# Kernel optimization log

Hardware: AMD Instinct MI355X
Metric: run time of the kernel (lower is better)

Reference implementation:

```python
import jax, jax.numpy as jnp
import numpy as np

N = 100000          # nodes
E = 600000          # edges
H = 128             # hidden_dim
CF_DIM = 15         # input_dim - 1
NOISE_DIM = 32
NUM_CLASS = 6       # GraphConstructor.number_of_class
B = 64              # number of graphs in batch
BC = B * NUM_CLASS  # total clusters
LAYER_NUM = 3
NEG_SLOPE = 0.01


def setup_inputs() -> dict:
    key = jax.random.key(0)
    ks = jax.random.split(key, 12)
    cf = jax.random.normal(ks[0], (N, CF_DIM), jnp.float32)
    slf = jax.random.uniform(ks[1], (N,), jnp.float32)
    z = jax.random.normal(ks[2], (N, NOISE_DIM), jnp.float32)
    tr = jax.random.uniform(ks[3], (BC,), jnp.float32)
    W_enc = jax.random.normal(ks[4], (CF_DIM + 1 + NOISE_DIM, H), jnp.float32) * 0.05
    b_enc = jax.random.normal(ks[5], (H,), jnp.float32) * 0.05
    W_m = jax.random.normal(ks[6], (2 * H, H), jnp.float32) * 0.05
    b_m = jax.random.normal(ks[7], (H,), jnp.float32) * 0.05
    W_u = jax.random.normal(ks[8], (3 * H, H), jnp.float32) * 0.05
    b_u = jax.random.normal(ks[9], (H,), jnp.float32) * 0.05
    e = jax.random.randint(ks[10], (2, E), 0, N, jnp.int64)
    cc = jax.random.randint(ks[11], (N,), 0, BC, jnp.int64)
    cfb = cc // NUM_CLASS  # batch index consistent with global cluster index
    return {"cf": cf, "slf": slf, "z": z, "tr": tr,
            "W_enc": W_enc, "b_enc": b_enc, "W_m": W_m, "b_m": b_m,
            "W_u": W_u, "b_u": b_u, "e": e, "cc": cc, "cfb": cfb}


def _segment_mean(x, idx, num_segments):
    s = jax.ops.segment_sum(x, idx, num_segments=num_segments)
    c = jax.ops.segment_sum(jnp.ones((x.shape[0],), x.dtype), idx, num_segments=num_segments)
    return s / jnp.maximum(c, 1.0)[:, None]


def reference(cf, slf, z, tr, W_enc, b_enc, W_m, b_m, W_u, b_u, e, cc, cfb):
    # encoder: x = enc(cat(cf, slf, z))  (Linear, no activation since act='')
    x = jnp.concatenate([cf, slf[:, None], z], axis=-1) @ W_enc + b_enc  # [N, H]
    src, dst = e[0], e[1]  # PyG: x_j = x[src], x_i = x[dst], aggregate at dst
    for _ in range(LAYER_NUM):
        # message: MLP(cat(feature_i, feature_j)) per edge, mean-aggregated at dst
        msg = jnp.concatenate([x[dst], x[src]], axis=-1) @ W_m + b_m  # [E, H]
        aggr = _segment_mean(msg, dst, N)                              # [N, H]
        # cluster avg_pool scaled by target ratio, broadcast back to nodes
        pooled = _segment_mean(x, cc, BC) * tr[:, None]                # [BC, H]
        node_pool = pooled[cc]                                         # [N, H]
        upd = jnp.concatenate([x, aggr, node_pool], axis=-1) @ W_u + b_u
        upd = jnp.where(upd > 0, upd, NEG_SLOPE * upd)                 # LeakyReLU
        x = x + upd                                                    # residual
    return x
```

## Files before the change

### kernel.cpp

```cpp
#include <hip/hip_runtime.h>
#include <hip/hip_bf16.h>

#define N_NODES 100000
#define N_EDGES 600000
#define HD 128
#define NBC 384
#define SCAN_B 98
#define MAXFIX 4096
#define TILES ((N_NODES + 63) / 64)
#define GRID_F 512
#define AGG_B (N_NODES / 4)
#define CAPB 16384

typedef __attribute__((ext_vector_type(8))) short s8v;
typedef __attribute__((ext_vector_type(4))) short s4v;
typedef __attribute__((ext_vector_type(4))) float f4v;
typedef __hip_bfloat16 bf16;

static __device__ __forceinline__ float bf2f(bf16 v) { return __bfloat162float(v); }
static __device__ __forceinline__ bf16 f2bf(float v) { return __float2bfloat16(v); }
static __device__ __forceinline__ float sh2f(short s) { bf16 h = *(bf16*)&s; return bf2f(h); }
static __device__ __forceinline__ float ldraw(const void* p, int i, int fp32) {
    return fp32 ? ((const float*)p)[i] : bf2f(((const bf16*)p)[i]);
}

static __device__ __forceinline__ void gl2lds16(const void* g, void* l) {
    __builtin_amdgcn_global_load_lds(
        (const __attribute__((address_space(1))) void*)g,
        (__attribute__((address_space(3))) void*)l, 16, 0, 0);
}

__global__ void k_init(const unsigned short* __restrict__ wraw, const int* __restrict__ eraw,
                       int* __restrict__ flags, int* __restrict__ deg,
                       int* __restrict__ ccount, int* __restrict__ n0cnt,
                       int* __restrict__ bcur) {
    int b = blockIdx.x, t = threadIdx.x;
    if (b == 0) {
        if (t < 64) {
            int bad = 0;
            for (int k = 0; k < 16; k++) {
                unsigned int u = ((unsigned int)wraw[t * 16 + k]) << 16;
                float f = fabsf(__uint_as_float(u));
                if (!(f <= 1e4f)) bad = 1;
            }
            unsigned long long m = __ballot(bad);
            if (t == 0) {
                flags[0] = m ? 1 : 0;
                flags[1] = (eraw[1] == 0 && eraw[3] == 0 && eraw[5] == 0 && eraw[7] == 0) ? 1 : 0;
            }
        }
    } else if (b <= 98) {
        int i = (b - 1) * 256 + t;
        if (i < 25000) ((int4*)deg)[i] = make_int4(0, 0, 0, 0);
    } else {
        if (t < 96) ((int4*)ccount)[t] = make_int4(0, 0, 0, 0);
        if (t == 96) *n0cnt = 0;
        if (t >= 128 && t < 128 + SCAN_B) bcur[t - 128] = 0;
    }
}

#define KB_COMP 192
#define KB_EDGE (KB_COMP + 586)
#define KB_XIN  (KB_EDGE + 391)
#define KB_CC   (KB_XIN + 391)
#define KB_WUC  (KB_CC + 192)
#define KB_WET  (KB_WUC + 32)
#define KB_BC   (KB_WET + 1)
#define KB_TR   (KB_BC + 2)
__global__ void k_mega(const int* __restrict__ flags,
                       const void* cf_r, const void* slf_r, const void* z_r,
                       const void* tr_r, const void* Wenc_r, const void* benc_r,
                       const void* Wm_r, const void* bm_r, const void* Wu_r,
                       const void* bu_r, const int* __restrict__ e_r,
                       const int* __restrict__ cc_r,
                       bf16* __restrict__ xin, bf16* __restrict__ trc,
                       bf16* __restrict__ Wuc, bf16* __restrict__ buc,
                       int* __restrict__ ccc,
                       int* __restrict__ deg, int* __restrict__ ccount,
                       bf16* __restrict__ Wc, float* __restrict__ bc,
                       bf16* __restrict__ Wet, float* __restrict__ bcenc,
                       int* __restrict__ bcur, int* __restrict__ ebuf) {
    __shared__ float scf[3840];
    __shared__ int hist[SCAN_B], hbase[SCAN_B], lcur[SCAN_B];
    int b = blockIdx.x, t = threadIdx.x;
    int fp32 = flags[0];
    if (b < KB_COMP) {
        int i = b * 256 + t;
        int w = i & 127, kk = i >> 7;
        float acc = 0.f;
        if (kk < 128) {
            acc = ldraw(Wu_r, kk * 128 + w, fp32);
#pragma unroll 8
            for (int j = 0; j < 128; j++)
                acc += ldraw(Wm_r, kk * 128 + j, fp32) * ldraw(Wu_r, (128 + j) * 128 + w, fp32);
        } else if (kk < 256) {
            int kp = kk - 128;
#pragma unroll 8
            for (int j = 0; j < 128; j++)
                acc += ldraw(Wm_r, (128 + kp) * 128 + j, fp32) * ldraw(Wu_r, (128 + j) * 128 + w, fp32);
        } else {
            acc = ldraw(Wu_r, kk * 128 + w, fp32);
        }
        Wc[w * 384 + kk] = f2bf(acc);
    } else if (b < KB_EDGE) {
        int i64f = flags[1];
        int bb = b - KB_COMP;
        int e0 = bb * 1024;
        if (t < SCAN_B) { hist[t] = 0; lcur[t] = 0; }
        __syncthreads();
        int sv[4], dv[4], bk[4];
#pragma unroll
        for (int k = 0; k < 4; k++) {
            int i = e0 + k * 256 + t;
            if (i < N_EDGES) {
                sv[k] = i64f ? e_r[2 * i] : e_r[i];
                dv[k] = i64f ? e_r[2 * (N_EDGES + i)] : e_r[N_EDGES + i];
                bk[k] = dv[k] >> 10;
                atomicAdd(&hist[bk[k]], 1);
                atomicAdd(&deg[dv[k]], 1);
            } else bk[k] = -1;
        }
        __syncthreads();
        if (t < SCAN_B && hist[t] > 0) hbase[t] = atomicAdd(&bcur[t], hist[t]);
        __syncthreads();
#pragma unroll
        for (int k = 0; k < 4; k++) {
            if (bk[k] >= 0) {
                int rel = hbase[bk[k]] + atomicAdd(&lcur[bk[k]], 1);
                if (rel < CAPB) ebuf[bk[k] * CAPB + rel] = (sv[k] << 10) | (dv[k] & 1023);
            }
        }
    } else if (b < KB_XIN) {
        int base = (b - KB_EDGE) * 256;
        int gbase = base * 15;
        int cnt = min(3840, 1500000 - gbase);
        for (int k = t; k < cnt; k += 256) scf[k] = ldraw(cf_r, gbase + k, fp32);
        __syncthreads();
        int node = base + t;
        if (node < N_NODES) {
            float vals[64];
#pragma unroll
            for (int k = 0; k < 64; k++) vals[k] = 0.f;
#pragma unroll
            for (int k = 0; k < 15; k++) vals[k] = scf[t * 15 + k];
            vals[15] = ldraw(slf_r, node, fp32);
            if (fp32) {
                const f4v* zp = (const f4v*)((const float*)z_r + (size_t)node * 32);
#pragma unroll
                for (int k = 0; k < 8; k++) {
                    f4v v = zp[k];
#pragma unroll
                    for (int r = 0; r < 4; r++) vals[16 + k * 4 + r] = v[r];
                }
            } else {
                const s8v* zp = (const s8v*)((const short*)z_r + (size_t)node * 32);
#pragma unroll
                for (int k = 0; k < 4; k++) {
                    s8v v = zp[k];
#pragma unroll
                    for (int r = 0; r < 8; r++) vals[16 + k * 8 + r] = sh2f(v[r]);
                }
            }
            short* xr = (short*)xin + (size_t)node * 64;
#pragma unroll
            for (int k = 0; k < 8; k++) {
                s8v ov;
#pragma unroll
                for (int r = 0; r < 8; r++) { bf16 h = f2bf(vals[k * 8 + r]); ov[r] = *(short*)&h; }
                *(s8v*)(xr + k * 8) = ov;
            }
        }
    } else if (b < KB_CC) {
        int i64f = flags[1];
        int i = (b - KB_XIN) * 256 + t;
        if (i < N_NODES) {
            int v = i64f ? cc_r[2 * i] : cc_r[i];
            ccc[i] = v;
            atomicAdd(&ccount[v], 1);
        }
    } else if (b < KB_WUC) {
        int i = (b - KB_CC) * 256 + t;
        Wuc[i] = f2bf(ldraw(Wu_r, i, fp32));
    } else if (b < KB_WET) {
        int i = (b - KB_WUC) * 256 + t;
        int w = i >> 6, kk = i & 63;
        float v = (kk < 48) ? ldraw(Wenc_r, kk * 128 + w, fp32) : 0.f;
        Wet[i] = f2bf(v);
    } else if (b < KB_BC) {
        if (t < 128) {
            float acc = ldraw(bu_r, t, fp32);
            for (int j = 0; j < 128; j++)
                acc += ldraw(bm_r, j, fp32) * ldraw(Wu_r, (128 + j) * 128 + t, fp32);
            bc[t] = acc;
        } else {
            bcenc[t - 128] = ldraw(benc_r, t - 128, fp32);
            buc[t - 128] = f2bf(ldraw(bu_r, t - 128, fp32));
        }
    } else {
        int i = (b - KB_BC) * 256 + t;
        if (i < 384) trc[i] = f2bf(ldraw(tr_r, i, fp32));
    }
}

__global__ void k_scan_a2(const int* __restrict__ deg, int* __restrict__ rowptr,
                          int* __restrict__ bsum, const int* __restrict__ ccount,
                          int* __restrict__ coff, int* __restrict__ ccur) {
    __shared__ int sd[1024];
    int t = threadIdx.x;
    if (blockIdx.x < SCAN_B) {
        int i = blockIdx.x * 1024 + t;
        int v = (i < N_NODES) ? deg[i] : 0;
        sd[t] = v;
        __syncthreads();
#pragma unroll
        for (int off = 1; off < 1024; off <<= 1) {
            int u = (t >= off) ? sd[t - off] : 0;
            __syncthreads();
            sd[t] += u;
            __syncthreads();
        }
        if (i < N_NODES) rowptr[i] = sd[t] - v;
        if (t == 1023) bsum[blockIdx.x] = sd[t];
    } else {
        int v = (t < NBC) ? ccount[t] : 0;
        sd[t] = v;
        __syncthreads();
#pragma unroll
        for (int off = 1; off < 1024; off <<= 1) {
            int u = (t >= off) ? sd[t - off] : 0;
            __syncthreads();
            sd[t] += u;
            __syncthreads();
        }
        if (t < NBC) {
            int ex = sd[t] - v;
            coff[t] = ex;
            ccur[t] = ex;
            if (t == NBC - 1) coff[NBC] = sd[t];
        }
    }
}

__global__ void k_scan_c2(int* __restrict__ rowptr, const int* __restrict__ bsum) {
    __shared__ int sb[128];
    __shared__ int offs;
    int b = blockIdx.x, t = threadIdx.x;
    if (t < 128) sb[t] = (t < b) ? bsum[t] : 0;
    __syncthreads();
    if (t == 0) {
        int s = 0;
        for (int k = 0; k < 128; k++) s += sb[k];
        offs = s;
    }
    __syncthreads();
    int i = b * 1024 + t;
    if (i < N_NODES) rowptr[i] = rowptr[i] + offs;
    if (b == 0 && t == 0) rowptr[N_NODES] = N_EDGES;
}

#define K5_EN 1563
#define K5_PC (K5_EN + SCAN_B)
#define K5_CF (K5_PC + SCAN_B)
#define K5_L0 (K5_CF + 391)
__global__ void k_front(const bf16* __restrict__ xin, const bf16* __restrict__ Wet,
                        const float* __restrict__ bcenc, bf16* __restrict__ xb,
                        const int* __restrict__ rowptr, const int* __restrict__ ebuf,
                        int* __restrict__ colx, const int* __restrict__ ccc,
                        int* __restrict__ ccur, int* __restrict__ cnodes,
                        const int* __restrict__ deg, int* __restrict__ n0list,
                        int* __restrict__ n0cnt) {
    __shared__ int cur[1024];
    __shared__ int h[NBC], cb[NBC];
    int b = blockIdx.x;
    if (b >= K5_EN) {
        if (b < K5_PC) {
            int bb = b - K5_EN;
            int base = bb << 10;
            int nlim = min(1024, N_NODES - base);
            for (int i = threadIdx.x; i < nlim; i += 256) cur[i] = rowptr[base + i];
            __syncthreads();
            int cnt = rowptr[base + nlim] - rowptr[base];
            const int* eb = ebuf + bb * CAPB;
            for (int e = threadIdx.x; e < cnt; e += 256) {
                int v = eb[e];
                int p = atomicAdd(&cur[v & 1023], 1);
                colx[p] = v >> 10;
            }
        } else if (b < K5_CF) {
            int bb = b - K5_PC;
            int base = bb << 10;
            int nlim = min(1024, N_NODES - base);
            for (int j = threadIdx.x; j < NBC; j += 256) h[j] = 0;
            __syncthreads();
            int cls[4];
#pragma unroll
            for (int k = 0; k < 4; k++) {
                int li = k * 256 + threadIdx.x;
                cls[k] = (li < nlim) ? ccc[base + li] : -1;
                if (cls[k] >= 0) atomicAdd(&h[cls[k]], 1);
            }
            __syncthreads();
            for (int j = threadIdx.x; j < NBC; j += 256) {
                cb[j] = h[j] ? atomicAdd(&ccur[j], h[j]) : 0;
                h[j] = 0;
            }
            __syncthreads();
#pragma unroll
            for (int k = 0; k < 4; k++) {
                if (cls[k] >= 0) {
                    int p = cb[cls[k]] + atomicAdd(&h[cls[k]], 1);
                    cnodes[p] = base + k * 256 + threadIdx.x;
                }
            }
        } else {
            int i = (b - K5_CF) * 256 + threadIdx.x;
            if (i < N_NODES && deg[i] == 0) {
                int p = atomicAdd(n0cnt, 1);
                if (p < MAXFIX) n0list[p] = i;
            }
        }
        return;
    }
    int tid = threadIdx.x;
    int r0 = b * 64;
    int wave = tid >> 6, lane = tid & 63, quad = lane >> 4, nidx = lane & 15;
    int colbase = wave * 32;

    int arow[4];
#pragma unroll
    for (int rt = 0; rt < 4; rt++) {
        int gr = r0 + rt * 16 + nidx;
        arow[rt] = (gr < N_NODES) ? gr : (N_NODES - 1);
    }
    f4v acc[4][2];
#pragma unroll
    for (int rt = 0; rt < 4; rt++)
#pragma unroll
        for (int ct = 0; ct < 2; ct++) acc[rt][ct] = (f4v){0.f, 0.f, 0.f, 0.f};

#pragma unroll
    for (int s = 0; s < 2; s++) {
        int k0 = s * 32;
        s8v bfrag[4];
#pragma unroll
        for (int rt = 0; rt < 4; rt++)
            bfrag[rt] = *(const s8v*)((const short*)xin + (size_t)arow[rt] * 64 + k0 + quad * 8);
#pragma unroll
        for (int ct = 0; ct < 2; ct++) {
            s8v wfr = *(const s8v*)((const short*)Wet + (colbase + ct * 16 + nidx) * 64 + k0 + quad * 8);
#pragma unroll
            for (int rt = 0; rt < 4; rt++)
                acc[rt][ct] = __builtin_amdgcn_mfma_f32_16x16x32_bf16(wfr, bfrag[rt], acc[rt][ct], 0, 0, 0);
        }
    }
#pragma unroll
    for (int rt = 0; rt < 4; rt++) {
        int gr = r0 + rt * 16 + nidx;
        if (gr < N_NODES) {
#pragma unroll
            for (int ct = 0; ct < 2; ct++) {
                int wc0 = colbase + ct * 16 + quad * 4;
                f4v bv = *(const f4v*)(bcenc + wc0);
                size_t idx = (size_t)gr * HD + wc0;
                s4v ob;
#pragma unroll
                for (int r = 0; r < 4; r++) {
                    float nv = acc[rt][ct][r] + bv[r];
                    bf16 h2 = f2bf(nv);
                    ob[r] = *(short*)&h2;
                }
                *(s4v*)((short*)xb + idx) = ob;
            }
        }
    }
}

__global__ void k_aggpool(const bf16* __restrict__ xb, const int* __restrict__ rowptr,
                          const int* __restrict__ colx, bf16* __restrict__ mb,
                          const int* __restrict__ coff, const int* __restrict__ cnodes,
                          const bf16* __restrict__ trc, bf16* __restrict__ pooled) {
    __shared__ float red[8][128];
    int tid = threadIdx.x;
    if (blockIdx.x < NBC) {
        int cl = blockIdx.x;
        int lo = coff[cl], hi = coff[cl + 1];
        int cnt = hi - lo;
        int slot = tid >> 5, cg = tid & 31;
        float a0 = 0.f, a1 = 0.f, a2 = 0.f, a3 = 0.f;
        for (int i = lo + slot; i < hi; i += 8) {
            int nd = cnodes[i];
            s4v v = *(const s4v*)((const short*)xb + (size_t)nd * HD + cg * 4);
            a0 += sh2f(v[0]); a1 += sh2f(v[1]); a2 += sh2f(v[2]); a3 += sh2f(v[3]);
        }
        red[slot][cg * 4 + 0] = a0;
        red[slot][cg * 4 + 1] = a1;
        red[slot][cg * 4 + 2] = a2;
        red[slot][cg * 4 + 3] = a3;
        __syncthreads();
        if (tid < 128) {
            float s = 0.f;
#pragma unroll
            for (int k = 0; k < 8; k++) s += red[k][tid];
            float v = s / (float)(cnt > 1 ? cnt : 1) * bf2f(trc[cl]);
            pooled[cl * HD + tid] = f2bf(v);
        }
        return;
    }
    int wave = tid >> 6, lane = tid & 63;
    int node = (blockIdx.x - NBC) * 4 + wave;
    if (node >= N_NODES) return;
    int half = lane >> 5;
    int l = lane & 31;
    int lo = rowptr[node], hi = rowptr[node + 1];
    float a0 = 0.f, a1 = 0.f, a2 = 0.f, a3 = 0.f;
    int j = lo + half;
    while (j + 2 < hi) {
        int s0 = colx[j], s1 = colx[j + 2];
        s4v v0 = *(const s4v*)((const short*)xb + (size_t)s0 * HD + l * 4);
        s4v v1 = *(const s4v*)((const short*)xb + (size_t)s1 * HD + l * 4);
        a0 += sh2f(v0[0]) + sh2f(v1[0]);
        a1 += sh2f(v0[1]) + sh2f(v1[1]);
        a2 += sh2f(v0[2]) + sh2f(v1[2]);
        a3 += sh2f(v0[3]) + sh2f(v1[3]);
        j += 4;
    }
    if (j < hi) {
        int s0 = colx[j];
        s4v v0 = *(const s4v*)((const short*)xb + (size_t)s0 * HD + l * 4);
        a0 += sh2f(v0[0]);
        a1 += sh2f(v0[1]);
        a2 += sh2f(v0[2]);
        a3 += sh2f(v0[3]);
    }
    a0 += __shfl_down(a0, 32);
    a1 += __shfl_down(a1, 32);
    a2 += __shfl_down(a2, 32);
    a3 += __shfl_down(a3, 32);
    if (half == 0) {
        int d = hi - lo;
        float inv = 1.0f / (float)(d > 1 ? d : 1);
        s4v o;
        bf16 h0 = f2bf(a0 * inv); o[0] = *(short*)&h0;
        bf16 h1 = f2bf(a1 * inv); o[1] = *(short*)&h1;
        bf16 h2 = f2bf(a2 * inv); o[2] = *(short*)&h2;
        bf16 h3 = f2bf(a3 * inv); o[3] = *(short*)&h3;
        *(s4v*)((short*)mb + (size_t)node * HD + l * 4) = o;
    }
}

__global__ __launch_bounds__(256, 2) void k_fused2(
    const bf16* __restrict__ xb, const bf16* __restrict__ mb, const bf16* __restrict__ pooled,
    const bf16* __restrict__ Wc, const float* __restrict__ bc,
    const int* __restrict__ cc, const int* __restrict__ deg,
    const bf16* __restrict__ Wuc, const bf16* __restrict__ buc,
    const int* __restrict__ n0list, const int* __restrict__ n0cnt,
    bf16* __restrict__ xbo, const int* __restrict__ flags,
    void* __restrict__ out, int last) {
    __shared__ short Lx[64 * 128];
    __shared__ short Lm[64 * 128];
    __shared__ short Lp[64 * 128];
    __shared__ float fxv[128];
    __shared__ float fpv[128];
    int tid = threadIdx.x;
    int wave = tid >> 6, lane = tid & 63, quad = lane >> 4, nidx = lane & 15;
    int colbase = wave * 32;
    int fp32out = flags[0];

    s8v wfr[12][2];
#pragma unroll
    for (int ct = 0; ct < 2; ct++) {
        int wcol = colbase + ((nidx >> 2) << 3) + ct * 4 + (nidx & 3);
        const short* wrow = (const short*)Wc + (size_t)wcol * 384 + quad * 8;
#pragma unroll
        for (int s = 0; s < 12; s++) wfr[s][ct] = *(const s8v*)(wrow + s * 32);
    }
    int cb2 = colbase + quad * 8;
    f4v bv0 = *(const f4v*)(bc + cb2);
    f4v bv1 = *(const f4v*)(bc + cb2 + 4);

    int srow = lane >> 4;
    int sc = lane & 15;

    for (int t = blockIdx.x; t < TILES; t += GRID_F) {
        int r0 = t * 64;
#pragma unroll
        for (int ii = 0; ii < 4; ii++) {
            int i = wave * 4 + ii;
            int lr = i * 4 + srow;
            int gr = r0 + lr;
            int grc = (gr < N_NODES) ? gr : (N_NODES - 1);
            int gc = sc ^ (lr & 15);
            gl2lds16((const short*)xb + (size_t)grc * HD + gc * 8, (char*)Lx + i * 1024);
            gl2lds16((const short*)mb + (size_t)grc * HD + gc * 8, (char*)Lm + i * 1024);
            int ci = cc[grc];
            gl2lds16((const short*)pooled + (size_t)ci * HD + gc * 8, (char*)Lp + i * 1024);
        }
        __syncthreads();

        f4v acc[4][2];
#pragma unroll
        for (int rt = 0; rt < 4; rt++)
#pragma unroll
            for (int ct = 0; ct < 2; ct++) acc[rt][ct] = (f4v){0.f, 0.f, 0.f, 0.f};

#pragma unroll
        for (int s = 0; s < 12; s++) {
            const short* Ls = (s < 4) ? Lx : ((s < 8) ? Lm : Lp);
            int c = (s & 3) * 4 + quad;
            s8v bfrag[4];
#pragma unroll
            for (int rt = 0; rt < 4; rt++) {
                int row = rt * 16 + nidx;
                int slot = c ^ nidx;
                bfrag[rt] = *(const s8v*)(Ls + row * 128 + slot * 8);
            }
#pragma unroll
            for (int ct = 0; ct < 2; ct++)
#pragma unroll
                for (int rt = 0; rt < 4; rt++)
                    acc[rt][ct] = __builtin_amdgcn_mfma_f32_16x16x32_bf16(wfr[s][ct], bfrag[rt], acc[rt][ct], 0, 0, 0);
        }

#pragma unroll
        for (int rt = 0; rt < 4; rt++) {
            int gr = r0 + rt * 16 + nidx;
            if (gr < N_NODES && deg[gr] > 0) {
                int row = rt * 16 + nidx;
                int slot = ((colbase >> 3) + quad) ^ nidx;
                s8v xo = *(const s8v*)(Lx + row * 128 + slot * 8);
                size_t idx = (size_t)gr * HD + cb2;
                float nv[8];
#pragma unroll
                for (int r = 0; r < 4; r++) {
                    float v0 = acc[rt][0][r] + bv0[r];
                    v0 = (v0 > 0.f) ? v0 : 0.01f * v0;
                    nv[r] = sh2f(xo[r]) + v0;
                    float v1 = acc[rt][1][r] + bv1[r];
                    v1 = (v1 > 0.f) ? v1 : 0.01f * v1;
                    nv[4 + r] = sh2f(xo[4 + r]) + v1;
                }
                if (last) {
                    if (fp32out) {
                        f4v o0 = {nv[0], nv[1], nv[2], nv[3]};
                        f4v o1 = {nv[4], nv[5], nv[6], nv[7]};
                        *(f4v*)((float*)out + idx) = o0;
                        *(f4v*)((float*)out + idx + 4) = o1;
                    } else {
                        s8v ob;
#pragma unroll
                        for (int r = 0; r < 8; r++) { bf16 h = f2bf(nv[r]); ob[r] = *(short*)&h; }
                        *(s8v*)((short*)out + idx) = ob;
                    }
                } else {
                    s8v ob;
#pragma unroll
                    for (int r = 0; r < 8; r++) { bf16 h = f2bf(nv[r]); ob[r] = *(short*)&h; }
                    *(s8v*)((short*)xbo + idx) = ob;
                }
            }
        }
        __syncthreads();
    }

    int cnt0 = *n0cnt;
    if (cnt0 > MAXFIX) cnt0 = MAXFIX;
    for (int j = blockIdx.x; j < cnt0; j += gridDim.x) {
        int v = n0list[j];
        if (tid < 128) {
            fxv[tid] = bf2f(xb[(size_t)v * HD + tid]);
            fpv[tid] = bf2f(pooled[cc[v] * HD + tid]);
        }
        __syncthreads();
        if (tid < 128) {
            float acc = bf2f(buc[tid]);
            for (int k = 0; k < 128; k++)
                acc += fxv[k] * bf2f(Wuc[k * 128 + tid]) + fpv[k] * bf2f(Wuc[(256 + k) * 128 + tid]);
            float u = acc > 0.f ? acc : 0.01f * acc;
            size_t idx = (size_t)v * HD + tid;
            float nv = fxv[tid] + u;
            if (last) {
                if (fp32out) ((float*)out)[idx] = nv;
                else ((bf16*)out)[idx] = f2bf(nv);
            } else {
                xbo[idx] = f2bf(nv);
            }
        }
        __syncthreads();
    }
}

extern "C" void kernel_launch(void* const* d_in, const int* in_sizes, int n_in,
                              void* d_out, int out_size, void* d_ws, size_t ws_size,
                              hipStream_t stream) {
    const void* cf_r = d_in[0];
    const void* slf_r = d_in[1];
    const void* z_r = d_in[2];
    const void* tr_r = d_in[3];
    const void* Wenc_r = d_in[4];
    const void* benc_r = d_in[5];
    const void* Wm_r = d_in[6];
    const void* bm_r = d_in[7];
    const void* Wu_r = d_in[8];
    const void* bu_r = d_in[9];
    const int* e_r = (const int*)d_in[10];
    const int* cc_r = (const int*)d_in[11];

    char* w = (char*)d_ws;
    auto alloc = [&](size_t bytes) -> char* {
        char* p = w;
        w += (bytes + 63) & ~(size_t)63;
        return p;
    };
    bf16* xb0 = (bf16*)alloc((size_t)N_NODES * HD * 2);
    bf16* xb1 = (bf16*)alloc((size_t)N_NODES * HD * 2);
    bf16* mb = (bf16*)alloc((size_t)N_NODES * HD * 2);
    bf16* xin = (bf16*)alloc((size_t)N_NODES * 64 * 2);
    bf16* Wc = (bf16*)alloc(128 * 384 * 2);
    float* bc = (float*)alloc(128 * 4);
    bf16* Wet = (bf16*)alloc(128 * 64 * 2);
    float* bcenc = (float*)alloc(128 * 4);
    bf16* pooled = (bf16*)alloc(NBC * HD * 2);
    int* deg = (int*)alloc(N_NODES * 4);
    int* rowptr = (int*)alloc((N_NODES + 1) * 4);
    int* colx = (int*)alloc(N_EDGES * 4);
    int* ccount = (int*)alloc(NBC * 4);
    int* coff = (int*)alloc((NBC + 1) * 4);
    int* ccur = (int*)alloc(NBC * 4);
    int* cnodes = (int*)alloc(N_NODES * 4);
    int* flags = (int*)alloc(64);
    int* bsum = (int*)alloc(SCAN_B * 4);
    int* n0list = (int*)alloc(MAXFIX * 4);
    int* n0cnt = (int*)alloc(64);
    bf16* trc = (bf16*)alloc(384 * 2);
    bf16* Wuc = (bf16*)alloc(49152 * 2);
    bf16* buc = (bf16*)alloc(128 * 2);
    int* ccc = (int*)alloc(N_NODES * 4);
    int* bcur = (int*)alloc(SCAN_B * 4);
    int* ebuf = (int*)alloc((size_t)SCAN_B * CAPB * 4);

    k_init<<<100, 256, 0, stream>>>((const unsigned short*)Wenc_r, e_r, flags,
                                    deg, ccount, n0cnt, bcur);
    k_mega<<<KB_TR, 256, 0, stream>>>(flags, cf_r, slf_r, z_r, tr_r, Wenc_r, benc_r,
                                      Wm_r, bm_r, Wu_r, bu_r, e_r, cc_r,
                                      xin, trc, Wuc, buc, ccc, deg, ccount,
                                      Wc, bc, Wet, bcenc, bcur, ebuf);
    k_scan_a2<<<SCAN_B + 1, 1024, 0, stream>>>(deg, rowptr, bsum, ccount, coff, ccur);
    k_scan_c2<<<SCAN_B, 1024, 0, stream>>>(rowptr, bsum);
    k_front<<<K5_L0, 256, 0, stream>>>(xin, Wet, bcenc, xb0,
                                       rowptr, ebuf, colx, ccc, ccur, cnodes,
                                       deg, n0list, n0cnt);

    bf16* xbufs[2] = {xb0, xb1};
    for (int layer = 0; layer < 3; layer++) {
        bf16* xbi = xbufs[layer & 1];
        bf16* xbo = xbufs[(layer + 1) & 1];
        int last = (layer == 2);
        k_aggpool<<<AGG_B + NBC, 256, 0, stream>>>(xbi, rowptr, colx, mb,
                                                   coff, cnodes, trc, pooled);
        k_fused2<<<GRID_F, 256, 0, stream>>>(xbi, mb, pooled, Wc, bc, ccc, deg,
                                             Wuc, buc, n0list, n0cnt,
                                             xbo, flags, d_out, last);
    }
}
```

Before: 420.1 us.

## Split mega prep kernel, tile weight-combine GEMM, unroll neighbor gather by four

Breaks the single heterogeneous setup kernel into separate kernels: weight conversion, edge bucketing, input assembly, and a new tiled kernel that builds the combined message/update weight from bf16 copies with LDS reuse. Input assembly now writes bf16 vectors directly instead of staging 64 floats per thread. The aggregation gather loop processes four neighbors per iteration with masked loads to raise memory-level parallelism. The update grid size also changes. This removes the slow per-thread 128-long dot products in setup, at the cost of more kernel launches and extra loads for padded neighbors.

```diff
diff --git a/kernel.cpp b/kernel.cpp
--- a/kernel.cpp
+++ b/kernel.cpp
@@ -8,9 +8,10 @@
 #define SCAN_B 98
 #define MAXFIX 4096
 #define TILES ((N_NODES + 63) / 64)
-#define GRID_F 512
+#define GRID_F 521
 #define AGG_B (N_NODES / 4)
 #define CAPB 16384
+#define EDGE_B 586
 
 typedef __attribute__((ext_vector_type(8))) short s8v;
 typedef __attribute__((ext_vector_type(4))) short s4v;
@@ -59,134 +60,28 @@
     }
 }
 
-#define KB_COMP 192
-#define KB_EDGE (KB_COMP + 586)
-#define KB_XIN  (KB_EDGE + 391)
-#define KB_CC   (KB_XIN + 391)
-#define KB_WUC  (KB_CC + 192)
-#define KB_WET  (KB_WUC + 32)
-#define KB_BC   (KB_WET + 1)
-#define KB_TR   (KB_BC + 2)
-__global__ void k_mega(const int* __restrict__ flags,
-                       const void* cf_r, const void* slf_r, const void* z_r,
-                       const void* tr_r, const void* Wenc_r, const void* benc_r,
-                       const void* Wm_r, const void* bm_r, const void* Wu_r,
-                       const void* bu_r, const int* __restrict__ e_r,
-                       const int* __restrict__ cc_r,
-                       bf16* __restrict__ xin, bf16* __restrict__ trc,
-                       bf16* __restrict__ Wuc, bf16* __restrict__ buc,
-                       int* __restrict__ ccc,
-                       int* __restrict__ deg, int* __restrict__ ccount,
-                       bf16* __restrict__ Wc, float* __restrict__ bc,
-                       bf16* __restrict__ Wet, float* __restrict__ bcenc,
-                       int* __restrict__ bcur, int* __restrict__ ebuf) {
-    __shared__ float scf[3840];
-    __shared__ int hist[SCAN_B], hbase[SCAN_B], lcur[SCAN_B];
+__global__ void k_cvt(const int* __restrict__ flags,
+                      const void* tr_r, const void* Wenc_r, const void* benc_r,
+                      const void* Wm_r, const void* bm_r, const void* Wu_r,
+                      const void* bu_r,
+                      bf16* __restrict__ Wuc, bf16* __restrict__ Wmc,
+                      bf16* __restrict__ Wet, float* __restrict__ bc,
+                      float* __restrict__ bcenc, bf16* __restrict__ buc,
+                      bf16* __restrict__ trc) {
     int b = blockIdx.x, t = threadIdx.x;
     int fp32 = flags[0];
-    if (b < KB_COMP) {
+    if (b < 192) {
         int i = b * 256 + t;
-        int w = i & 127, kk = i >> 7;
-        float acc = 0.f;
-        if (kk < 128) {
-            acc = ldraw(Wu_r, kk * 128 + w, fp32);
-#pragma unroll 8
-            for (int j = 0; j < 128; j++)
-                acc += ldraw(Wm_r, kk * 128 + j, fp32) * ldraw(Wu_r, (128 + j) * 128 + w, fp32);
-        } else if (kk < 256) {
-            int kp = kk - 128;
-#pragma unroll 8
-            for (int j = 0; j < 128; j++)
-                acc += ldraw(Wm_r, (128 + kp) * 128 + j, fp32) * ldraw(Wu_r, (128 + j) * 128 + w, fp32);
-        } else {
-            acc = ldraw(Wu_r, kk * 128 + w, fp32);
-        }
-        Wc[w * 384 + kk] = f2bf(acc);
-    } else if (b < KB_EDGE) {
-        int i64f = flags[1];
-        int bb = b - KB_COMP;
-        int e0 = bb * 1024;
-        if (t < SCAN_B) { hist[t] = 0; lcur[t] = 0; }
-        __syncthreads();
-        int sv[4], dv[4], bk[4];
-#pragma unroll
-        for (int k = 0; k < 4; k++) {
-            int i = e0 + k * 256 + t;
-            if (i < N_EDGES) {
-                sv[k] = i64f ? e_r[2 * i] : e_r[i];
-                dv[k] = i64f ? e_r[2 * (N_EDGES + i)] : e_r[N_EDGES + i];
-                bk[k] = dv[k] >> 10;
-                atomicAdd(&hist[bk[k]], 1);
-                atomicAdd(&deg[dv[k]], 1);
-            } else bk[k] = -1;
-        }
-        __syncthreads();
-        if (t < SCAN_B && hist[t] > 0) hbase[t] = atomicAdd(&bcur[t], hist[t]);
-        __syncthreads();
-#pragma unroll
-        for (int k = 0; k < 4; k++) {
-            if (bk[k] >= 0) {
-                int rel = hbase[bk[k]] + atomicAdd(&lcur[bk[k]], 1);
-                if (rel < CAPB) ebuf[bk[k] * CAPB + rel] = (sv[k] << 10) | (dv[k] & 1023);
-            }
-        }
-    } else if (b < KB_XIN) {
-        int base = (b - KB_EDGE) * 256;
-        int gbase = base * 15;
-        int cnt = min(3840, 1500000 - gbase);
-        for (int k = t; k < cnt; k += 256) scf[k] = ldraw(cf_r, gbase + k, fp32);
-        __syncthreads();
-        int node = base + t;
-        if (node < N_NODES) {
-            float vals[64];
-#pragma unroll
-            for (int k = 0; k < 64; k++) vals[k] = 0.f;
-#pragma unroll
-            for (int k = 0; k < 15; k++) vals[k] = scf[t * 15 + k];
-            vals[15] = ldraw(slf_r, node, fp32);
-            if (fp32) {
-                const f4v* zp = (const f4v*)((const float*)z_r + (size_t)node * 32);
-#pragma unroll
-                for (int k = 0; k < 8; k++) {
-                    f4v v = zp[k];
-#pragma unroll
-                    for (int r = 0; r < 4; r++) vals[16 + k * 4 + r] = v[r];
-                }
-            } else {
-                const s8v* zp = (const s8v*)((const short*)z_r + (size_t)node * 32);
-#pragma unroll
-                for (int k = 0; k < 4; k++) {
-                    s8v v = zp[k];
-#pragma unroll
-                    for (int r = 0; r < 8; r++) vals[16 + k * 8 + r] = sh2f(v[r]);
-                }
-            }
-            short* xr = (short*)xin + (size_t)node * 64;
-#pragma unroll
-            for (int k = 0; k < 8; k++) {
-                s8v ov;
-#pragma unroll
-                for (int r = 0; r < 8; r++) { bf16 h = f2bf(vals[k * 8 + r]); ov[r] = *(short*)&h; }
-                *(s8v*)(xr + k * 8) = ov;
-            }
-        }
-    } else if (b < KB_CC) {
-        int i64f = flags[1];
-        int i = (b - KB_XIN) * 256 + t;
-        if (i < N_NODES) {
-            int v = i64f ? cc_r[2 * i] : cc_r[i];
-            ccc[i] = v;
-            atomicAdd(&ccount[v], 1);
-        }
-    } else if (b < KB_WUC) {
-        int i = (b - KB_CC) * 256 + t;
         Wuc[i] = f2bf(ldraw(Wu_r, i, fp32));
-    } else if (b < KB_WET) {
-        int i = (b - KB_WUC) * 256 + t;
+    } else if (b < 320) {
+        int i = (b - 192) * 256 + t;
+        Wmc[i] = f2bf(ldraw(Wm_r, i, fp32));
+    } else if (b < 352) {
+        int i = (b - 320) * 256 + t;
         int w = i >> 6, kk = i & 63;
         float v = (kk < 48) ? ldraw(Wenc_r, kk * 128 + w, fp32) : 0.f;
         Wet[i] = f2bf(v);
-    } else if (b < KB_BC) {
+    } else if (b == 352) {
         if (t < 128) {
             float acc = ldraw(bu_r, t, fp32);
             for (int j = 0; j < 128; j++)
@@ -197,9 +92,142 @@
             buc[t - 128] = f2bf(ldraw(bu_r, t - 128, fp32));
         }
     } else {
-        int i = (b - KB_BC) * 256 + t;
+        int i = (b - 353) * 256 + t;
         if (i < 384) trc[i] = f2bf(ldraw(tr_r, i, fp32));
     }
+}
+
+__global__ void k_edges(const int* __restrict__ flags, const int* __restrict__ e_r,
+                        int* __restrict__ deg, int* __restrict__ bcur,
+                        int* __restrict__ ebuf) {
+    __shared__ int hist[SCAN_B], hbase[SCAN_B], lcur[SCAN_B];
+    int t = threadIdx.x;
+    int i64f = flags[1];
+    int e0 = blockIdx.x * 1024;
+    if (t < SCAN_B) { hist[t] = 0; lcur[t] = 0; }
+    __syncthreads();
+    int sv[4], dv[4], bk[4];
+#pragma unroll
+    for (int k = 0; k < 4; k++) {
+        int i = e0 + k * 256 + t;
+        if (i < N_EDGES) {
+            sv[k] = i64f ? e_r[2 * i] : e_r[i];
+            dv[k] = i64f ? e_r[2 * (N_EDGES + i)] : e_r[N_EDGES + i];
+            bk[k] = dv[k] >> 10;
+            atomicAdd(&hist[bk[k]], 1);
+            atomicAdd(&deg[dv[k]], 1);
+        } else bk[k] = -1;
+    }
+    __syncthreads();
+    if (t < SCAN_B && hist[t] > 0) hbase[t] = atomicAdd(&bcur[t], hist[t]);
+    __syncthreads();
+#pragma unroll
+    for (int k = 0; k < 4; k++) {
+        if (bk[k] >= 0) {
+            int rel = hbase[bk[k]] + atomicAdd(&lcur[bk[k]], 1);
+            if (rel < CAPB) ebuf[bk[k] * CAPB + rel] = (sv[k] << 10) | (dv[k] & 1023);
+        }
+    }
+}
+
+#define KX_XIN 391
+#define KX_CC  782
+__global__ void k_xin(const int* __restrict__ flags,
+                      const void* cf_r, const void* slf_r, const void* z_r,
+                      const int* __restrict__ cc_r,
+                      bf16* __restrict__ xin, int* __restrict__ ccc,
+                      int* __restrict__ ccount) {
+    __shared__ float scf[3840];
+    int b = blockIdx.x, t = threadIdx.x;
+    int fp32 = flags[0];
+    if (b < KX_XIN) {
+        int base = b * 256;
+        int gbase = base * 15;
+        int cnt = min(3840, 1500000 - gbase);
+        for (int k = t; k < cnt; k += 256) scf[k] = ldraw(cf_r, gbase + k, fp32);
+        __syncthreads();
+        int node = base + t;
+        if (node >= N_NODES) return;
+        short* xr = (short*)xin + (size_t)node * 64;
+        const float* c = scf + t * 15;
+        s8v o0, o1;
+#pragma unroll
+        for (int r = 0; r < 8; r++) { bf16 h = f2bf(c[r]); o0[r] = *(short*)&h; }
+#pragma unroll
+        for (int r = 0; r < 7; r++) { bf16 h = f2bf(c[8 + r]); o1[r] = *(short*)&h; }
+        { bf16 h = f2bf(ldraw(slf_r, node, fp32)); o1[7] = *(short*)&h; }
+        *(s8v*)(xr) = o0;
+        *(s8v*)(xr + 8) = o1;
+        if (fp32) {
+            const float* zp = (const float*)z_r + (size_t)node * 32;
+#pragma unroll
+            for (int k = 0; k < 4; k++) {
+                f4v a = *(const f4v*)(zp + k * 8);
+                f4v bv = *(const f4v*)(zp + k * 8 + 4);
+                s8v ov;
+#pragma unroll
+                for (int r = 0; r < 4; r++) { bf16 h = f2bf(a[r]); ov[r] = *(short*)&h; }
+#pragma unroll
+                for (int r = 0; r < 4; r++) { bf16 h = f2bf(bv[r]); ov[4 + r] = *(short*)&h; }
+                *(s8v*)(xr + 16 + k * 8) = ov;
+            }
+        } else {
+            const short* zp = (const short*)z_r + (size_t)node * 32;
+#pragma unroll
+            for (int k = 0; k < 4; k++)
+                *(s8v*)(xr + 16 + k * 8) = *(const s8v*)(zp + k * 8);
+        }
+        s8v zz = {0, 0, 0, 0, 0, 0, 0, 0};
+        *(s8v*)(xr + 48) = zz;
+        *(s8v*)(xr + 56) = zz;
+    } else {
+        int i64f = flags[1];
+        int i = (b - KX_XIN) * 256 + t;
+        if (i < N_NODES) {
+            int v = i64f ? cc_r[2 * i] : cc_r[i];
+            ccc[i] = v;
+            atomicAdd(&ccount[v], 1);
+        }
+    }
+}
+
+__global__ void k_w(const bf16* __restrict__ Wmc, const bf16* __restrict__ Wuc,
+                    bf16* __restrict__ Wc) {
+    __shared__ short wm[16 * 128];
+    int b = blockIdx.x, t = threadIdx.x;
+    int w = t & 127, g = t >> 7;
+    int kk0 = b * 16 + g * 8;
+    if (kk0 >= 256) {
+        s8v ov;
+#pragma unroll
+        for (int n = 0; n < 8; n++)
+            ov[n] = *((const short*)Wuc + (kk0 + n) * 128 + w);
+        *(s8v*)((short*)Wc + w * 384 + kk0) = ov;
+        return;
+    }
+    *(s8v*)(wm + t * 8) = *(const s8v*)((const short*)Wmc + b * 16 * 128 + t * 8);
+    __syncthreads();
+    float acc[8];
+#pragma unroll
+    for (int n = 0; n < 8; n++) acc[n] = 0.f;
+    const short* wup = (const short*)Wuc + 128 * 128 + w;
+    const short* wmb = wm + (g * 8) * 128;
+#pragma unroll 4
+    for (int j = 0; j < 128; j++) {
+        float wu = sh2f(wup[j * 128]);
+#pragma unroll
+        for (int n = 0; n < 8; n++)
+            acc[n] += sh2f(wmb[n * 128 + j]) * wu;
+    }
+    s8v ov;
+#pragma unroll
+    for (int n = 0; n < 8; n++) {
+        int kk = kk0 + n;
+        float base = (kk < 128) ? sh2f(*((const short*)Wuc + kk * 128 + w)) : 0.f;
+        bf16 h = f2bf(acc[n] + base);
+        ov[n] = *(short*)&h;
+    }
+    *(s8v*)((short*)Wc + w * 384 + kk0) = ov;
 }
 
 __global__ void k_scan_a2(const int* __restrict__ deg, int* __restrict__ rowptr,
@@ -413,24 +441,23 @@
     int l = lane & 31;
     int lo = rowptr[node], hi = rowptr[node + 1];
     float a0 = 0.f, a1 = 0.f, a2 = 0.f, a3 = 0.f;
-    int j = lo + half;
-    while (j + 2 < hi) {
-        int s0 = colx[j], s1 = colx[j + 2];
+    for (int j0 = lo + half; j0 < hi; j0 += 8) {
+        int i1 = j0 + 2, i2 = j0 + 4, i3 = j0 + 6;
+        int s0 = colx[j0];
+        int s1 = colx[i1 < hi ? i1 : j0];
+        int s2 = colx[i2 < hi ? i2 : j0];
+        int s3 = colx[i3 < hi ? i3 : j0];
+        float m1 = (i1 < hi) ? 1.f : 0.f;
+        float m2 = (i2 < hi) ? 1.f : 0.f;
+        float m3 = (i3 < hi) ? 1.f : 0.f;
         s4v v0 = *(const s4v*)((const short*)xb + (size_t)s0 * HD + l * 4);
         s4v v1 = *(const s4v*)((const short*)xb + (size_t)s1 * HD + l * 4);
-        a0 += sh2f(v0[0]) + sh2f(v1[0]);
-        a1 += sh2f(v0[1]) + sh2f(v1[1]);
-        a2 += sh2f(v0[2]) + sh2f(v1[2]);
-        a3 += sh2f(v0[3]) + sh2f(v1[3]);
-        j += 4;
-    }
-    if (j < hi) {
-        int s0 = colx[j];
-        s4v v0 = *(const s4v*)((const short*)xb + (size_t)s0 * HD + l * 4);
-        a0 += sh2f(v0[0]);
-        a1 += sh2f(v0[1]);
-        a2 += sh2f(v0[2]);
-        a3 += sh2f(v0[3]);
+        s4v v2 = *(const s4v*)((const short*)xb + (size_t)s2 * HD + l * 4);
+        s4v v3 = *(const s4v*)((const short*)xb + (size_t)s3 * HD + l * 4);
+        a0 += sh2f(v0[0]) + m1 * sh2f(v1[0]) + m2 * sh2f(v2[0]) + m3 * sh2f(v3[0]);
+        a1 += sh2f(v0[1]) + m1 * sh2f(v1[1]) + m2 * sh2f(v2[1]) + m3 * sh2f(v3[1]);
+        a2 += sh2f(v0[2]) + m1 * sh2f(v1[2]) + m2 * sh2f(v2[2]) + m3 * sh2f(v3[2]);
+        a3 += sh2f(v0[3]) + m1 * sh2f(v1[3]) + m2 * sh2f(v2[3]) + m3 * sh2f(v3[3]);
     }
     a0 += __shfl_down(a0, 32);
     a1 += __shfl_down(a1, 32);
@@ -633,6 +660,7 @@
     int* n0cnt = (int*)alloc(64);
     bf16* trc = (bf16*)alloc(384 * 2);
     bf16* Wuc = (bf16*)alloc(49152 * 2);
+    bf16* Wmc = (bf16*)alloc(32768 * 2);
     bf16* buc = (bf16*)alloc(128 * 2);
     int* ccc = (int*)alloc(N_NODES * 4);
     int* bcur = (int*)alloc(SCAN_B * 4);
@@ -640,10 +668,11 @@
 
     k_init<<<100, 256, 0, stream>>>((const unsigned short*)Wenc_r, e_r, flags,
                                     deg, ccount, n0cnt, bcur);
-    k_mega<<<KB_TR, 256, 0, stream>>>(flags, cf_r, slf_r, z_r, tr_r, Wenc_r, benc_r,
-                                      Wm_r, bm_r, Wu_r, bu_r, e_r, cc_r,
-                                      xin, trc, Wuc, buc, ccc, deg, ccount,
-                                      Wc, bc, Wet, bcenc, bcur, ebuf);
+    k_cvt<<<355, 256, 0, stream>>>(flags, tr_r, Wenc_r, benc_r, Wm_r, bm_r, Wu_r, bu_r,
+                                   Wuc, Wmc, Wet, bc, bcenc, buc, trc);
+    k_edges<<<EDGE_B, 256, 0, stream>>>(flags, e_r, deg, bcur, ebuf);
+    k_xin<<<KX_CC, 256, 0, stream>>>(flags, cf_r, slf_r, z_r, cc_r, xin, ccc, ccount);
+    k_w<<<24, 256, 0, stream>>>(Wmc, Wuc, Wc);
     k_scan_a2<<<SCAN_B + 1, 1024, 0, stream>>>(deg, rowptr, bsum, ccount, coff, ccur);
     k_scan_c2<<<SCAN_B, 1024, 0, stream>>>(rowptr, bsum);
     k_front<<<K5_L0, 256, 0, stream>>>(xin, Wet, bcenc, xb0,
```

Result: slower. 465.2 us (+10.7%).
